# Kernel optimization log

Measured on AMD Instinct MI355X. Metric: run time of the kernel, lower is better.

The kernel has to match this reference:

```python
import jax, jax.numpy as jnp
import numpy as np
from jax import lax

EPS = 1e-5

def binarize(x):
    # sign forward, straight-through (identity) backward, matching torch .data-trick Binarize
    return x + lax.stop_gradient(jnp.sign(x) - x)

def conv2d(x, w, pad):
    return lax.conv_general_dilated(x, w, window_strides=(1, 1),
                                    padding=[(pad, pad), (pad, pad)],
                                    dimension_numbers=('NCHW', 'OIHW', 'NCHW'))

def maxpool_k2s1(x):
    return lax.reduce_window(x, -jnp.inf, lax.max, (1, 1, 2, 2), (1, 1, 1, 1), 'VALID')

def batchnorm(x, g, b):
    # training-mode BN: batch statistics over (N, H, W)
    mean = jnp.mean(x, axis=(0, 2, 3), keepdims=True)
    var = jnp.var(x, axis=(0, 2, 3), keepdims=True)
    return (x - mean) * lax.rsqrt(var + EPS) * g[None, :, None, None] + b[None, :, None, None]

def hardtanh(x):
    return jnp.clip(x, -1.0, 1.0)

def setup_inputs() -> dict:
    key = jax.random.key(0)
    ks = jax.random.split(key, 11)
    B = 4096
    return {
        'x':   jax.random.normal(ks[0], (B, 12, 12, 15), jnp.float32),
        'w1':  jax.random.normal(ks[1], (48, 12, 3, 3), jnp.float32) * 0.1,
        'g1':  1.0 + 0.1 * jax.random.normal(ks[2], (48,), jnp.float32),
        'b1':  0.1 * jax.random.normal(ks[3], (48,), jnp.float32),
        'w2':  jax.random.normal(ks[4], (48, 48, 3, 3), jnp.float32) * 0.1,
        'g2':  1.0 + 0.1 * jax.random.normal(ks[5], (48,), jnp.float32),
        'b2':  0.1 * jax.random.normal(ks[6], (48,), jnp.float32),
        'w3':  jax.random.normal(ks[7], (48, 48, 3, 3), jnp.float32) * 0.1,
        'g3':  1.0 + 0.1 * jax.random.normal(ks[8], (48,), jnp.float32),
        'b3':  0.1 * jax.random.normal(ks[9], (48,), jnp.float32),
        'wfc': jax.random.normal(ks[10], (5, 54 * 48), jnp.float32) * 0.02,
    }

def reference(x, w1, g1, b1, w2, g2, b2, w3, g3, b3, wfc):
    # BinarizeConv2d binarizes activations (in_channels != 3) and weights; returns binarized input too
    xb1 = binarize(x)                                  # [B,12,12,15]
    h = conv2d(xb1, binarize(w1), pad=1)               # [B,48,12,15]
    h = maxpool_k2s1(h)                                # [B,48,11,14]
    h = hardtanh(batchnorm(h, g1, b1))
    xb2 = binarize(h)
    h = conv2d(xb2, binarize(w2), pad=0)               # [B,48,9,12]
    h = hardtanh(batchnorm(h, g2, b2))
    xb3 = binarize(h)
    h = conv2d(xb3, binarize(w3), pad=0)               # [B,48,7,10]
    h = maxpool_k2s1(h)                                # [B,48,6,9] -> 54 spatial
    h = hardtanh(batchnorm(h, g3, b3))
    f = h.reshape(h.shape[0], -1)                      # [B, 2592]
    fb = binarize(f)
    out = fb @ binarize(wfc).T                         # [B, 5]  (LogSoftmax defined but never applied)
    return (out, xb1, xb2, xb3, fb)
```

## Files before the change

### kernel.cpp

```cpp
#include <hip/hip_runtime.h>
#include <stdint.h>

typedef unsigned long long u64;
typedef unsigned int u32;
typedef unsigned short u16;
typedef unsigned char u8;
typedef signed char s8;

#define NB 4096

#define WS_STATS 0
#define WS_W1Q   20480
#define WS_W2P   24576
#define WS_W3P   28672
#define WS_WFCP  32768
#define WS_A2    40960
#define WS_P1    5087232

#define OUT_OFF 0
#define XB1_OFF 20480
#define XB2_OFF 8867840
#define XB3_OFF 39145472
#define FB_OFF  60379136

__device__ __forceinline__ float fsign(float v) {
    return (v > 0.0f) ? 1.0f : ((v < 0.0f) ? -1.0f : 0.0f);
}
__device__ __forceinline__ int sb8(int v, int k) {
    return (int)(s8)(v >> (8*k));
}
__device__ __forceinline__ int sh16(int v, int h) {
    return h ? (v >> 16) : (int)(short)v;
}

__global__ __launch_bounds__(512)
void kw_pack(const float* __restrict__ w1, const float* __restrict__ w2,
             const float* __restrict__ w3, const float* __restrict__ wfc,
             u32* __restrict__ W1Q, u64* __restrict__ W2P, u64* __restrict__ W3P,
             u64* __restrict__ WFCP, long long* __restrict__ stats) {
    int t = threadIdx.x;
    for (int i = t; i < 2304; i += 512) stats[i] = 0;
    if (t < 48) {
        u16 m1[9];
        #pragma unroll
        for (int p = 0; p < 9; ++p) {
            u16 m = 0;
            for (int c = 0; c < 12; ++c)
                if (w1[t*108 + c*9 + p] > 0.0f) m |= (u16)(1u << c);
            m1[p] = m;
        }
        #pragma unroll
        for (int j = 0; j < 4; ++j)
            W1Q[t*5 + j] = (u32)m1[2*j] | ((u32)m1[2*j+1] << 16);
        W1Q[t*5 + 4] = (u32)m1[8];
    }
    if (t < 432) {
        int oc = t / 9, p = t % 9;
        u64 m2 = 0, m3 = 0;
        for (int c = 0; c < 48; ++c) {
            if (w2[oc*432 + c*9 + p] > 0.0f) m2 |= (1ull << c);
            if (w3[oc*432 + c*9 + p] > 0.0f) m3 |= (1ull << c);
        }
        W2P[t] = m2;
        W3P[t] = m3;
    }
    if (t < 205) {
        int o = t / 41, j = t % 41;
        u64 m = 0;
        for (int l = 0; l < 64; ++l) {
            int k = j*64 + l;
            if (k < 2592 && wfc[o*2592 + k] > 0.0f) m |= (1ull << l);
        }
        WFCP[t] = m;
    }
}

__global__ __launch_bounds__(192)
void k1(const float* __restrict__ x, const u32* __restrict__ W1Q,
        float* __restrict__ dout, u8* __restrict__ P1g, u64* __restrict__ stats) {
    __shared__ u16 As[180];
    __shared__ int cmap[2304];
    __shared__ int2 part[192];
    int t = threadIdx.x, b = blockIdx.x;
    if (t < 180) {
        const float* xp = x + b*2160 + t;
        float* xo = dout + XB1_OFF + (size_t)b*2160 + t;
        u16 m = 0;
        #pragma unroll
        for (int c = 0; c < 12; ++c) {
            float v = xp[c*180];
            xo[c*180] = fsign(v);
            if (v > 0.0f) m |= (u16)(1u << c);
        }
        As[t] = m;
    }
    __syncthreads();
    if (t < 180) {
        int y = t / 15, xx = t % 15;
        u16 tap[9], msk[9];
        int nv = 0;
        #pragma unroll
        for (int ky = 0; ky < 3; ++ky) {
            #pragma unroll
            for (int kx = 0; kx < 3; ++kx) {
                int yy = y + ky - 1, xc = xx + kx - 1;
                bool v = (yy >= 0 && yy < 12 && xc >= 0 && xc < 15);
                int yl = min(max(yy, 0), 11), xl = min(max(xc, 0), 14);
                tap[ky*3+kx] = As[yl*15 + xl];
                msk[ky*3+kx] = v ? (u16)0xFFFF : (u16)0;
                nv += v ? 12 : 0;
            }
        }
        u32 tq[5], mq[5];
        #pragma unroll
        for (int j = 0; j < 4; ++j) {
            tq[j] = (u32)tap[2*j] | ((u32)tap[2*j+1] << 16);
            mq[j] = (u32)msk[2*j] | ((u32)msk[2*j+1] << 16);
        }
        tq[4] = tap[8]; mq[4] = msk[8];
        s8* cb = (s8*)cmap;
        #pragma unroll 4
        for (int oc = 0; oc < 48; ++oc) {
            int acc = 0;
            #pragma unroll
            for (int j = 0; j < 5; ++j)
                acc += __popc((tq[j] ^ W1Q[oc*5 + j]) & mq[j]);
            cb[oc*192 + y*16 + xx] = (s8)(nv - 2*acc);
        }
    }
    __syncthreads();
    {
        int c = t >> 2, q = t & 3;
        int r0 = 3*q, nr = (q < 3) ? 3 : 2;
        int rowv[4][4];
        #pragma unroll
        for (int j = 0; j < 4; ++j)
            if (j <= nr) {
                #pragma unroll
                for (int i = 0; i < 4; ++i)
                    rowv[j][i] = cmap[c*48 + (r0 + j)*4 + i];
            }
        int sum = 0, sq = 0;
        u8* gp = P1g + (size_t)b*8448 + c*176;
        #pragma unroll
        for (int pr = 0; pr < 3; ++pr) {
            if (pr < nr) {
                int o0 = 0, o1 = 0, o2 = 0, o3 = 0;
                #pragma unroll
                for (int k = 0; k < 14; ++k) {
                    int a0 = sb8(rowv[pr][k>>2], k&3);
                    int a1 = sb8(rowv[pr][(k+1)>>2], (k+1)&3);
                    int b0 = sb8(rowv[pr+1][k>>2], k&3);
                    int b1 = sb8(rowv[pr+1][(k+1)>>2], (k+1)&3);
                    int mx = max(max(a0, a1), max(b0, b1));
                    sum += mx; sq += mx*mx;
                    int sh = 8*(k&3);
                    if ((k>>2) == 0) o0 |= (mx & 255) << sh;
                    else if ((k>>2) == 1) o1 |= (mx & 255) << sh;
                    else if ((k>>2) == 2) o2 |= (mx & 255) << sh;
                    else o3 |= (mx & 255) << sh;
                }
                *((int4*)(gp + (r0 + pr)*16)) = make_int4(o0, o1, o2, o3);
            }
        }
        part[t] = make_int2(sum, sq);
    }
    __syncthreads();
    if (t < 48) {
        int s = 0, q = 0;
        #pragma unroll
        for (int k = 0; k < 4; ++k) { s += part[t*4+k].x; q += part[t*4+k].y; }
        int slot = b & 7;
        atomicAdd(&stats[t*8 + slot],        (u64)(long long)s);
        atomicAdd(&stats[(48 + t)*8 + slot], (u64)(long long)q);
    }
}

__global__ __launch_bounds__(256)
void kA(const float* __restrict__ g1, const float* __restrict__ b1,
        const long long* __restrict__ statsIn, const int4* __restrict__ P1g4,
        float* __restrict__ dout, u64* __restrict__ A2,
        const u64* __restrict__ W2, u64* __restrict__ statsOut) {
    __shared__ float sc[48], sh[48];
    __shared__ int smP[2112];
    __shared__ u64 As[154];
    __shared__ short c2s[5184];
    __shared__ int2 part[192];
    int t = threadIdx.x, b = blockIdx.x;
    for (int i = t; i < 528; i += 256) ((int4*)smP)[i] = P1g4[(size_t)b*528 + i];
    if (t < 48) {
        long long s = 0, q = 0;
        #pragma unroll
        for (int k = 0; k < 8; ++k) { s += statsIn[t*8 + k]; q += statsIn[(48 + t)*8 + k]; }
        double N = 630784.0;
        double mean = (double)s / N;
        double var  = (double)q / N - mean*mean;
        double scale = (double)g1[t] / sqrt(var + 1e-5);
        sc[t] = (float)scale;
        sh[t] = (float)((double)b1[t] - mean*scale);
    }
    __syncthreads();
    const s8* smb = (const s8*)smP;
    float4* xo = (float4*)(dout + XB2_OFF + (size_t)b*7392);
    for (int i4 = t; i4 < 462; i4 += 256) {
        int i = 4*i4;
        float r[4];
        #pragma unroll
        for (int k = 0; k < 4; ++k) {
            int idx = i + k;
            int c = idx / 154, s = idx - 154*c;
            int row = s / 14, px = s - 14*row;
            int v = smb[c*176 + row*16 + px];
            r[k] = fsign(sc[c]*(float)v + sh[c]);
        }
        float4 o; o.x = r[0]; o.y = r[1]; o.z = r[2]; o.w = r[3];
        xo[i4] = o;
    }
    if (t < 154) {
        int row = t / 14, px = t - 14*row;
        int po = row*16 + px;
        u64 m = 0;
        #pragma unroll
        for (int c = 0; c < 48; ++c)
            if (sc[c]*(float)smb[c*176 + po] + sh[c] > 0.0f) m |= (1ull << c);
        As[t] = m;
        A2[(size_t)b*154 + t] = m;
    }
    __syncthreads();
    if (t < 216) {
        int pos = (t < 108) ? t : (t - 108);
        int ocb = (t < 108) ? 0 : 24;
        int oy = pos / 12, ox = pos - 12*oy;
        u64 tap[9];
        #pragma unroll
        for (int ky = 0; ky < 3; ++ky)
            #pragma unroll
            for (int kx = 0; kx < 3; ++kx)
                tap[ky*3+kx] = As[(oy+ky)*14 + ox + kx];
        #pragma unroll 4
        for (int oc = ocb; oc < ocb + 24; ++oc) {
            int acc = 0;
            #pragma unroll
            for (int k = 0; k < 9; ++k)
                acc += __popcll(tap[k] ^ W2[oc*9 + k]);
            c2s[oc*108 + pos] = (short)(432 - 2*acc);
        }
    }
    __syncthreads();
    if (t < 192) {
        int c = t >> 2, q = t & 3;
        const int* ci = (const int*)(c2s + c*108);
        int sum = 0, sq = 0;
        for (int j = q; j < 54; j += 4) {
            int v2 = ci[j];
            int lo = (int)(short)v2, hi = v2 >> 16;
            sum += lo + hi; sq += lo*lo + hi*hi;
        }
        part[t] = make_int2(sum, sq);
    }
    __syncthreads();
    if (t < 48) {
        int s = 0, q = 0;
        #pragma unroll
        for (int k = 0; k < 4; ++k) { s += part[t*4+k].x; q += part[t*4+k].y; }
        int slot = b & 7;
        atomicAdd(&statsOut[(96 + t)*8 + slot],  (u64)(long long)s);
        atomicAdd(&statsOut[(144 + t)*8 + slot], (u64)(long long)q);
    }
}

__global__ __launch_bounds__(256)
void kB(const float* __restrict__ g2, const float* __restrict__ b2,
        const long long* __restrict__ statsIn, const u64* __restrict__ A2,
        const u64* __restrict__ W2, const u64* __restrict__ W3,
        float* __restrict__ dout, int* __restrict__ P3i,
        u64* __restrict__ statsOut) {
    __shared__ float sc[48], sh[48];
    __shared__ u64 As[154];
    __shared__ short c2s[5184];
    __shared__ u64 A3[108];
    __shared__ short cm[3360];
    __shared__ int2 part[192];
    int t = threadIdx.x, b = blockIdx.x;
    if (t < 154) As[t] = A2[(size_t)b*154 + t];
    if (t < 48) {
        long long s = 0, q = 0;
        #pragma unroll
        for (int k = 0; k < 8; ++k) { s += statsIn[(96 + t)*8 + k]; q += statsIn[(144 + t)*8 + k]; }
        double N = 442368.0;
        double mean = (double)s / N;
        double var  = (double)q / N - mean*mean;
        double scale = (double)g2[t] / sqrt(var + 1e-5);
        sc[t] = (float)scale;
        sh[t] = (float)((double)b2[t] - mean*scale);
    }
    __syncthreads();
    if (t < 216) {
        int pos = (t < 108) ? t : (t - 108);
        int ocb = (t < 108) ? 0 : 24;
        int oy = pos / 12, ox = pos - 12*oy;
        u64 tap[9];
        #pragma unroll
        for (int ky = 0; ky < 3; ++ky)
            #pragma unroll
            for (int kx = 0; kx < 3; ++kx)
                tap[ky*3+kx] = As[(oy+ky)*14 + ox + kx];
        #pragma unroll 4
        for (int oc = ocb; oc < ocb + 24; ++oc) {
            int acc = 0;
            #pragma unroll
            for (int k = 0; k < 9; ++k)
                acc += __popcll(tap[k] ^ W2[oc*9 + k]);
            c2s[oc*108 + pos] = (short)(432 - 2*acc);
        }
    }
    __syncthreads();
    float4* xo = (float4*)(dout + XB3_OFF + (size_t)b*5184);
    for (int i4 = t; i4 < 1296; i4 += 256) {
        int c = i4 / 27, s4 = i4 - 27*c;
        short4 v4 = *(const short4*)&c2s[c*108 + s4*4];
        float4 o;
        o.x = fsign(sc[c]*(float)v4.x + sh[c]);
        o.y = fsign(sc[c]*(float)v4.y + sh[c]);
        o.z = fsign(sc[c]*(float)v4.z + sh[c]);
        o.w = fsign(sc[c]*(float)v4.w + sh[c]);
        xo[i4] = o;
    }
    if (t < 108) {
        u64 m = 0;
        #pragma unroll
        for (int c = 0; c < 48; ++c)
            if (sc[c]*(float)c2s[c*108 + t] + sh[c] > 0.0f) m |= (1ull << c);
        A3[t] = m;
    }
    __syncthreads();
    if (t < 210) {
        int grp = (t < 70) ? 0 : ((t < 140) ? 1 : 2);
        int pos = t - grp*70;
        int ocb = grp*16;
        int oy = pos / 10, ox = pos - 10*oy;
        u64 tap[9];
        #pragma unroll
        for (int ky = 0; ky < 3; ++ky)
            #pragma unroll
            for (int kx = 0; kx < 3; ++kx)
                tap[ky*3+kx] = A3[(oy+ky)*12 + ox + kx];
        #pragma unroll 4
        for (int oc = ocb; oc < ocb + 16; ++oc) {
            int acc = 0;
            #pragma unroll
            for (int k = 0; k < 9; ++k)
                acc += __popcll(tap[k] ^ W3[oc*9 + k]);
            cm[oc*70 + pos] = (short)(432 - 2*acc);
        }
    }
    __syncthreads();
    {
        int c = t >> 2, q = t & 3;
        if (t < 192) {
            int pr0 = (q < 2) ? 2*q : (q + 2);
            int npr = (q < 2) ? 2 : 1;
            int rowv[3][5];
            const int* cmi = (const int*)(cm + c*70);
            #pragma unroll
            for (int j = 0; j < 3; ++j)
                if (j <= npr) {
                    #pragma unroll
                    for (int i = 0; i < 5; ++i)
                        rowv[j][i] = cmi[(pr0 + j)*5 + i];
                }
            int sum = 0, sq = 0;
            int* gp = P3i + (size_t)b*1440 + c*30;
            #pragma unroll
            for (int pr = 0; pr < 2; ++pr) {
                if (pr < npr) {
                    int o[5] = {0, 0, 0, 0, 0};
                    #pragma unroll
                    for (int k = 0; k < 9; ++k) {
                        int a0 = sh16(rowv[pr][k>>1], k&1);
                        int a1 = sh16(rowv[pr][(k+1)>>1], (k+1)&1);
                        int b0 = sh16(rowv[pr+1][k>>1], k&1);
                        int b1 = sh16(rowv[pr+1][(k+1)>>1], (k+1)&1);
                        int mx = max(max(a0, a1), max(b0, b1));
                        sum += mx; sq += mx*mx;
                        o[k>>1] |= (mx & 0xffff) << (16*(k&1));
                    }
                    #pragma unroll
                    for (int j = 0; j < 5; ++j) gp[(pr0 + pr)*5 + j] = o[j];
                }
            }
            part[t] = make_int2(sum, sq);
        }
    }
    __syncthreads();
    if (t < 48) {
        int s = 0, q = 0;
        #pragma unroll
        for (int k = 0; k < 4; ++k) { s += part[t*4+k].x; q += part[t*4+k].y; }
        int slot = b & 7;
        atomicAdd(&statsOut[(192 + t)*8 + slot], (u64)(long long)s);
        atomicAdd(&statsOut[(240 + t)*8 + slot], (u64)(long long)q);
    }
}

__global__ __launch_bounds__(256)
void kC(const float* __restrict__ g3, const float* __restrict__ b3,
        const long long* __restrict__ statsIn, const int4* __restrict__ P3g4,
        const u64* __restrict__ WFC, float* __restrict__ dout) {
    __shared__ float sc[48], sh[48];
    __shared__ int smP[1440];
    __shared__ u8 nib[648];
    __shared__ u64 fbb[41];
    int t = threadIdx.x, b = blockIdx.x;
    for (int i = t; i < 360; i += 256) ((int4*)smP)[i] = P3g4[(size_t)b*360 + i];
    if (t < 48) {
        long long s = 0, q = 0;
        #pragma unroll
        for (int k = 0; k < 8; ++k) { s += statsIn[(192 + t)*8 + k]; q += statsIn[(240 + t)*8 + k]; }
        double N = 221184.0;
        double mean = (double)s / N;
        double var  = (double)q / N - mean*mean;
        double scale = (double)g3[t] / sqrt(var + 1e-5);
        sc[t] = (float)scale;
        sh[t] = (float)((double)b3[t] - mean*scale);
    }
    __syncthreads();
    const short* smS = (const short*)smP;
    float4* fo = (float4*)(dout + FB_OFF + (size_t)b*2592);
    for (int i4 = t; i4 < 648; i4 += 256) {
        int i = 4*i4;
        float r[4];
        unsigned n = 0;
        #pragma unroll
        for (int k = 0; k < 4; ++k) {
            int idx = i + k;
            int c = idx / 54, s = idx - 54*c;
            int row = s / 9, px = s - 9*row;
            float bn = sc[c]*(float)smS[c*60 + row*10 + px] + sh[c];
            r[k] = fsign(bn);
            if (bn > 0.0f) n |= (1u << k);
        }
        float4 o; o.x = r[0]; o.y = r[1]; o.z = r[2]; o.w = r[3];
        fo[i4] = o;
        nib[i4] = (u8)n;
    }
    __syncthreads();
    if (t < 41) {
        u64 m = 0;
        #pragma unroll
        for (int k = 0; k < 16; ++k) {
            int j = t*16 + k;
            if (j < 648) m |= ((u64)nib[j]) << (4*k);
        }
        fbb[t] = m;
    }
    __syncthreads();
    if (t < 5) {
        const u64* Wf = WFC + t*41;
        int acc = 0;
        #pragma unroll
        for (int j = 0; j < 41; ++j) acc += __popcll(fbb[j] ^ Wf[j]);
        dout[OUT_OFF + b*5 + t] = (float)(2592 - 2*acc);
    }
}

extern "C" void kernel_launch(void* const* d_in, const int* in_sizes, int n_in,
                              void* d_out, int out_size, void* d_ws, size_t ws_size,
                              hipStream_t stream) {
    const float* x   = (const float*)d_in[0];
    const float* w1  = (const float*)d_in[1];
    const float* g1  = (const float*)d_in[2];
    const float* b1  = (const float*)d_in[3];
    const float* w2  = (const float*)d_in[4];
    const float* g2  = (const float*)d_in[5];
    const float* b2  = (const float*)d_in[6];
    const float* w3  = (const float*)d_in[7];
    const float* g3  = (const float*)d_in[8];
    const float* b3  = (const float*)d_in[9];
    const float* wfc = (const float*)d_in[10];
    float* out = (float*)d_out;
    char* ws = (char*)d_ws;

    long long* stats = (long long*)(ws + WS_STATS);
    u32*       W1Q   = (u32*)(ws + WS_W1Q);
    u64*       W2P   = (u64*)(ws + WS_W2P);
    u64*       W3P   = (u64*)(ws + WS_W3P);
    u64*       WFCP  = (u64*)(ws + WS_WFCP);
    u64*       A2    = (u64*)(ws + WS_A2);
    u8*        P1g   = (u8*)(ws + WS_P1);
    int*       P3i   = (int*)(ws + WS_P1);

    hipLaunchKernelGGL(kw_pack, dim3(1),  dim3(512), 0, stream,
                       w1, w2, w3, wfc, W1Q, W2P, W3P, WFCP, stats);
    hipLaunchKernelGGL(k1,      dim3(NB), dim3(192), 0, stream,
                       x, W1Q, out, P1g, (u64*)stats);
    hipLaunchKernelGGL(kA,      dim3(NB), dim3(256), 0, stream,
                       g1, b1, stats, (const int4*)P1g, out, A2, W2P, (u64*)stats);
    hipLaunchKernelGGL(kB,      dim3(NB), dim3(256), 0, stream,
                       g2, b2, stats, A2, W2P, W3P, out, P3i, (u64*)stats);
    hipLaunchKernelGGL(kC,      dim3(NB), dim3(256), 0, stream,
                       g3, b3, stats, (const int4*)P3i, WFCP, out);
}
```

Measured before the change: 618.4 us.

## Vectorize xb1 sign output and split xb2 output write into separate kernel

In k1 the input is now read and its sign written with contiguous float4 accesses, staging the positive-bit flags in shared memory before packing the per-pixel channel masks. The xb2 float output write moves out of kA into a new grid-stride kernel kS2, which recomputes the BN1 scale and shift and reads the pooled int8 map directly from global memory. kA no longer stages P1 in shared memory and reads bytes strided from global memory instead. The aim is coalesced stores and lighter per-block work in kA, at the cost of one extra launch and a second read of P1.

```diff
diff --git a/kernel.cpp b/kernel.cpp
--- a/kernel.cpp
+++ b/kernel.cpp
@@ -16,6 +16,7 @@
 #define WS_WFCP  32768
 #define WS_A2    40960
 #define WS_P1    5087232
+#define WS_P3    5087232
 
 #define OUT_OFF 0
 #define XB1_OFF 20480
@@ -25,9 +26,6 @@
 
 __device__ __forceinline__ float fsign(float v) {
     return (v > 0.0f) ? 1.0f : ((v < 0.0f) ? -1.0f : 0.0f);
-}
-__device__ __forceinline__ int sb8(int v, int k) {
-    return (int)(s8)(v >> (8*k));
 }
 __device__ __forceinline__ int sh16(int v, int h) {
     return h ? (v >> 16) : (int)(short)v;
@@ -78,20 +76,31 @@
 __global__ __launch_bounds__(192)
 void k1(const float* __restrict__ x, const u32* __restrict__ W1Q,
         float* __restrict__ dout, u8* __restrict__ P1g, u64* __restrict__ stats) {
+    __shared__ u8 bitsb[2160];
     __shared__ u16 As[180];
     __shared__ int cmap[2304];
     __shared__ int2 part[192];
     int t = threadIdx.x, b = blockIdx.x;
+    {
+        const float4* xp = (const float4*)(x + (size_t)b*2160);
+        float4* xo = (float4*)(dout + XB1_OFF + (size_t)b*2160);
+        for (int j = t; j < 540; j += 192) {
+            float4 v = xp[j];
+            float4 o;
+            o.x = fsign(v.x); o.y = fsign(v.y); o.z = fsign(v.z); o.w = fsign(v.w);
+            xo[j] = o;
+            bitsb[4*j]   = v.x > 0.0f;
+            bitsb[4*j+1] = v.y > 0.0f;
+            bitsb[4*j+2] = v.z > 0.0f;
+            bitsb[4*j+3] = v.w > 0.0f;
+        }
+    }
+    __syncthreads();
     if (t < 180) {
-        const float* xp = x + b*2160 + t;
-        float* xo = dout + XB1_OFF + (size_t)b*2160 + t;
         u16 m = 0;
         #pragma unroll
-        for (int c = 0; c < 12; ++c) {
-            float v = xp[c*180];
-            xo[c*180] = fsign(v);
-            if (v > 0.0f) m |= (u16)(1u << c);
-        }
+        for (int c = 0; c < 12; ++c)
+            m |= ((u16)bitsb[c*180 + t]) << c;
         As[t] = m;
     }
     __syncthreads();
@@ -148,17 +157,17 @@
                 int o0 = 0, o1 = 0, o2 = 0, o3 = 0;
                 #pragma unroll
                 for (int k = 0; k < 14; ++k) {
-                    int a0 = sb8(rowv[pr][k>>2], k&3);
-                    int a1 = sb8(rowv[pr][(k+1)>>2], (k+1)&3);
-                    int b0 = sb8(rowv[pr+1][k>>2], k&3);
-                    int b1 = sb8(rowv[pr+1][(k+1)>>2], (k+1)&3);
+                    int a0 = (int)(s8)(rowv[pr][k>>2] >> (8*(k&3)));
+                    int a1 = (int)(s8)(rowv[pr][(k+1)>>2] >> (8*((k+1)&3)));
+                    int b0 = (int)(s8)(rowv[pr+1][k>>2] >> (8*(k&3)));
+                    int b1 = (int)(s8)(rowv[pr+1][(k+1)>>2] >> (8*((k+1)&3)));
                     int mx = max(max(a0, a1), max(b0, b1));
                     sum += mx; sq += mx*mx;
-                    int sh = 8*(k&3);
-                    if ((k>>2) == 0) o0 |= (mx & 255) << sh;
-                    else if ((k>>2) == 1) o1 |= (mx & 255) << sh;
-                    else if ((k>>2) == 2) o2 |= (mx & 255) << sh;
-                    else o3 |= (mx & 255) << sh;
+                    int shl = 8*(k&3);
+                    if ((k>>2) == 0) o0 |= (mx & 255) << shl;
+                    else if ((k>>2) == 1) o1 |= (mx & 255) << shl;
+                    else if ((k>>2) == 2) o2 |= (mx & 255) << shl;
+                    else o3 |= (mx & 255) << shl;
                 }
                 *((int4*)(gp + (r0 + pr)*16)) = make_int4(o0, o1, o2, o3);
             }
@@ -178,16 +187,14 @@
 
 __global__ __launch_bounds__(256)
 void kA(const float* __restrict__ g1, const float* __restrict__ b1,
-        const long long* __restrict__ statsIn, const int4* __restrict__ P1g4,
-        float* __restrict__ dout, u64* __restrict__ A2,
-        const u64* __restrict__ W2, u64* __restrict__ statsOut) {
+        const long long* __restrict__ statsIn, const u8* __restrict__ P1g,
+        u64* __restrict__ A2, const u64* __restrict__ W2,
+        u64* __restrict__ statsOut) {
     __shared__ float sc[48], sh[48];
-    __shared__ int smP[2112];
     __shared__ u64 As[154];
     __shared__ short c2s[5184];
     __shared__ int2 part[192];
     int t = threadIdx.x, b = blockIdx.x;
-    for (int i = t; i < 528; i += 256) ((int4*)smP)[i] = P1g4[(size_t)b*528 + i];
     if (t < 48) {
         long long s = 0, q = 0;
         #pragma unroll
@@ -200,29 +207,13 @@
         sh[t] = (float)((double)b1[t] - mean*scale);
     }
     __syncthreads();
-    const s8* smb = (const s8*)smP;
-    float4* xo = (float4*)(dout + XB2_OFF + (size_t)b*7392);
-    for (int i4 = t; i4 < 462; i4 += 256) {
-        int i = 4*i4;
-        float r[4];
-        #pragma unroll
-        for (int k = 0; k < 4; ++k) {
-            int idx = i + k;
-            int c = idx / 154, s = idx - 154*c;
-            int row = s / 14, px = s - 14*row;
-            int v = smb[c*176 + row*16 + px];
-            r[k] = fsign(sc[c]*(float)v + sh[c]);
-        }
-        float4 o; o.x = r[0]; o.y = r[1]; o.z = r[2]; o.w = r[3];
-        xo[i4] = o;
-    }
     if (t < 154) {
         int row = t / 14, px = t - 14*row;
-        int po = row*16 + px;
+        const u8* pb = P1g + (size_t)b*8448 + row*16 + px;
         u64 m = 0;
         #pragma unroll
         for (int c = 0; c < 48; ++c)
-            if (sc[c]*(float)smb[c*176 + po] + sh[c] > 0.0f) m |= (1ull << c);
+            if (sc[c]*(float)(s8)pb[c*176] + sh[c] > 0.0f) m |= (1ull << c);
         As[t] = m;
         A2[(size_t)b*154 + t] = m;
     }
@@ -266,6 +257,47 @@
         int slot = b & 7;
         atomicAdd(&statsOut[(96 + t)*8 + slot],  (u64)(long long)s);
         atomicAdd(&statsOut[(144 + t)*8 + slot], (u64)(long long)q);
+    }
+}
+
+__global__ __launch_bounds__(256)
+void kS2(const float* __restrict__ g1, const float* __restrict__ b1,
+         const long long* __restrict__ statsIn, const u8* __restrict__ P1g,
+         float* __restrict__ dout) {
+    __shared__ float sc[48], sh[48];
+    int t = threadIdx.x;
+    if (t < 48) {
+        long long s = 0, q = 0;
+        #pragma unroll
+        for (int k = 0; k < 8; ++k) { s += statsIn[t*8 + k]; q += statsIn[(48 + t)*8 + k]; }
+        double N = 630784.0;
+        double mean = (double)s / N;
+        double var  = (double)q / N - mean*mean;
+        double scale = (double)g1[t] / sqrt(var + 1e-5);
+        sc[t] = (float)scale;
+        sh[t] = (float)((double)b1[t] - mean*scale);
+    }
+    __syncthreads();
+    float4* xo = (float4*)(dout + XB2_OFF);
+    int gid = blockIdx.x*256 + t;
+    for (int j = gid; j < 7569408; j += 1048576) {
+        int base = 4*j;
+        int b = base / 7392;
+        int u = base - 7392*b;
+        const u8* pb = P1g + (size_t)b*8448;
+        float r[4];
+        #pragma unroll
+        for (int k = 0; k < 4; ++k) {
+            int uk = u + k;
+            int c = uk / 154;
+            int s = uk - 154*c;
+            int row = s / 14;
+            int px = s - 14*row;
+            int v = (int)(s8)pb[c*176 + row*16 + px];
+            r[k] = fsign(sc[c]*(float)v + sh[c]);
+        }
+        float4 o; o.x = r[0]; o.y = r[1]; o.z = r[2]; o.w = r[3];
+        xo[j] = o;
     }
 }
 
@@ -488,16 +520,18 @@
     u64*       WFCP  = (u64*)(ws + WS_WFCP);
     u64*       A2    = (u64*)(ws + WS_A2);
     u8*        P1g   = (u8*)(ws + WS_P1);
-    int*       P3i   = (int*)(ws + WS_P1);
-
-    hipLaunchKernelGGL(kw_pack, dim3(1),  dim3(512), 0, stream,
+    int*       P3i   = (int*)(ws + WS_P3);
+
+    hipLaunchKernelGGL(kw_pack, dim3(1),    dim3(512), 0, stream,
                        w1, w2, w3, wfc, W1Q, W2P, W3P, WFCP, stats);
-    hipLaunchKernelGGL(k1,      dim3(NB), dim3(192), 0, stream,
+    hipLaunchKernelGGL(k1,      dim3(NB),   dim3(192), 0, stream,
                        x, W1Q, out, P1g, (u64*)stats);
-    hipLaunchKernelGGL(kA,      dim3(NB), dim3(256), 0, stream,
-                       g1, b1, stats, (const int4*)P1g, out, A2, W2P, (u64*)stats);
-    hipLaunchKernelGGL(kB,      dim3(NB), dim3(256), 0, stream,
+    hipLaunchKernelGGL(kA,      dim3(NB),   dim3(256), 0, stream,
+                       g1, b1, stats, P1g, A2, W2P, (u64*)stats);
+    hipLaunchKernelGGL(kS2,     dim3(NB),   dim3(256), 0, stream,
+                       g1, b1, stats, P1g, out);
+    hipLaunchKernelGGL(kB,      dim3(NB),   dim3(256), 0, stream,
                        g2, b2, stats, A2, W2P, W3P, out, P3i, (u64*)stats);
-    hipLaunchKernelGGL(kC,      dim3(NB), dim3(256), 0, stream,
+    hipLaunchKernelGGL(kC,      dim3(NB),   dim3(256), 0, stream,
                        g3, b3, stats, (const int4*)P3i, WFCP, out);
 }
```

After: 641.9 us. 1.04x slower.
